# Performance work log

Measured on AMD Instinct MI355X. Metric: run time of the kernel, lower is better.

Reference implementation:

```python
import jax, jax.numpy as jnp
import numpy as np

OPS = jnp.array([[1,1,1],[1,1,-1],[1,-1,1],[1,-1,-1],[-1,1,1],[-1,1,-1],[-1,-1,1],[-1,-1,-1]], dtype=jnp.float32)  # [8,3] sign flips per eigenvector column

B, N, FN, FE, E = 1, 512, 8, 1, 32
D0 = 6 + FN  # layer-0 node embedding dim: framed (x,v) = 6 dims + node features


def setup_inputs() -> dict:
    key = jax.random.key(0)
    ks = jax.random.split(key, 24)
    rn = lambda k, shp, s=0.1: jax.random.normal(k, shp, jnp.float32) * s
    inp = {
        'node_feat': jax.random.normal(ks[0], (B, N, FN), jnp.float32),
        'edge_feat': jax.random.normal(ks[1], (B, N, N, FE), jnp.float32),
        'x': jax.random.normal(ks[2], (B, N, 3), jnp.float32),
        'v': jax.random.normal(ks[3], (B, N, 3), jnp.float32),
        # GNN layer 0 (input node dim D0)
        'e0_w1': rn(ks[4], (FE + 2 * D0, E)), 'e0_b1': jnp.zeros((E,), jnp.float32),
        'e0_w2': rn(ks[5], (E, E)), 'e0_b2': jnp.zeros((E,), jnp.float32),
        'n0_w1': rn(ks[6], (D0 + E, E)), 'n0_b1': jnp.zeros((E,), jnp.float32),
        'n0_w2': rn(ks[7], (E, E)), 'n0_b2': jnp.zeros((E,), jnp.float32),
        # GNN layer 1 (input node dim E)
        'e1_w1': rn(ks[8], (FE + 2 * E, E)), 'e1_b1': jnp.zeros((E,), jnp.float32),
        'e1_w2': rn(ks[9], (E, E)), 'e1_b2': jnp.zeros((E,), jnp.float32),
        'n1_w1': rn(ks[10], (E + E, E)), 'n1_b1': jnp.zeros((E,), jnp.float32),
        'n1_w2': rn(ks[11], (E, E)), 'n1_b2': jnp.zeros((E,), jnp.float32),
        # decoder: relu -> Linear(E,E) -> relu -> Linear(E,6)
        'dec_w1': rn(ks[12], (E, E)), 'dec_b1': jnp.zeros((E,), jnp.float32),
        'dec_w2': rn(ks[13], (E, 6)), 'dec_b2': jnp.zeros((6,), jnp.float32),
        # v_coef: relu -> Linear(E,E) -> relu -> Linear(E,1)
        'vc_w1': rn(ks[14], (E, E)), 'vc_b1': jnp.zeros((E,), jnp.float32),
        'vc_w2': rn(ks[15], (E, 1)), 'vc_b2': jnp.zeros((1,), jnp.float32),
    }
    return inp


def _gnn_layer(h, edge_feat, ew1, eb1, ew2, eb2, nw1, nb1, nw2, nb2):
    # h: [B,N,d]; edge_feat: [B,N,N,Fe]
    # Torch builds concat([edge_feat, h_j, h_i]) per (i,j) pair; we split W1 rows
    # to avoid materializing the [B,N,N,Fe+2d] concat (same math).
    Fe = edge_feat.shape[-1]
    d = h.shape[-1]
    pre_e = edge_feat @ ew1[:Fe]          # [B,N,N,E]
    pre_j = h @ ew1[Fe:Fe + d]            # [B,N,E], indexed by j
    pre_i = h @ ew1[Fe + d:]              # [B,N,E], indexed by i
    m = jax.nn.relu(pre_e + pre_j[:, None, :, :] + pre_i[:, :, None, :] + eb1)
    m = jax.nn.relu(m @ ew2 + eb2)        # [B,N,N,E]
    agg = m.sum(axis=2)                   # sum over neighbors j -> [B,N,E]
    dn = jax.nn.relu(h @ nw1[:d] + agg @ nw1[d:] + nb1)
    return dn @ nw2 + nb2                 # [B,N,E]


def reference(node_feat, edge_feat, x, v,
              e0_w1, e0_b1, e0_w2, e0_b2, n0_w1, n0_b1, n0_w2, n0_b2,
              e1_w1, e1_b1, e1_w2, e1_b2, n1_w1, n1_b1, n1_w2, n1_b2,
              dec_w1, dec_b1, dec_w2, dec_b2, vc_w1, vc_b1, vc_w2, vc_b2):
    # ---- create_frame (PCA frame averaging) ----
    center = x.mean(axis=1, keepdims=True)                 # [B,1,3]
    xc = x - center
    R = jnp.einsum('bni,bnj->bij', xc, xc)                 # [B,3,3]
    _, Vv = jnp.linalg.eigh(R)                             # eigenvectors, ascending (like torch.symeig)
    F_ops = jax.lax.stop_gradient(OPS[None, :, None, :] * Vv[:, None, :, :])  # [B,8,3,3]
    center = jax.lax.stop_gradient(center)
    xc = x - center
    fx = jnp.einsum('boji,bnj->obni', F_ops, xc)           # [8,B,N,3] (F_ops^T applied)
    fv = jnp.einsum('boji,bnj->obni', F_ops, v)            # [8,B,N,3]
    nf = jnp.broadcast_to(node_feat[None], (8,) + node_feat.shape)
    h0 = jnp.concatenate([fx, fv, nf], axis=-1)            # [8,B,N,6+FN]

    l0 = (e0_w1, e0_b1, e0_w2, e0_b2, n0_w1, n0_b1, n0_w2, n0_b2)
    l1 = (e1_w1, e1_b1, e1_w2, e1_b2, n1_w1, n1_b1, n1_w2, n1_b2)
    frames = []
    for i in range(8):  # small fixed frame count; loop keeps N^2 intermediates per-frame
        hi = _gnn_layer(h0[i], edge_feat, *l0)
        hi = _gnn_layer(hi, edge_feat, *l1)
        frames.append(hi)
    h_out = jnp.stack(frames)                              # [8,B,N,E]

    # ---- decoder + invert_frame ----
    s = jax.nn.relu(jax.nn.relu(h_out) @ dec_w1 + dec_b1)
    spatial_out = s @ dec_w2 + dec_b2                      # [8,B,N,6]
    so = jnp.transpose(spatial_out, (1, 0, 2, 3))          # [B,8,N,6]
    dx = jnp.einsum('boij,bonj->bni', F_ops, so[..., :3]) / 8.0
    dv = jnp.einsum('boij,bonj->bni', F_ops, so[..., 3:]) / 8.0

    h_mean = h_out.mean(axis=0)                            # [B,N,E]
    coef = jax.nn.relu(jax.nn.relu(h_mean) @ vc_w1 + vc_b1) @ vc_w2 + vc_b2  # [B,N,1]
    v_out = v + dv
    x_out = x + v_out * coef + dx
    return (h_mean, edge_feat, x_out, v_out)
```

## Files before the change

### kernel.cpp

```cpp
#include <hip/hip_runtime.h>
#include <hip/hip_bf16.h>
#include <hip/hip_fp16.h>
#include <math.h>

#define NN 512

typedef _Float16 f16x8 __attribute__((ext_vector_type(8)));
typedef float    f32x4 __attribute__((ext_vector_type(4)));

__device__ __forceinline__ void compute_frame(const float* __restrict__ x,
                                              float* __restrict__ sFR,
                                              double (*red)[9]) {
    const int t = threadIdx.x;
    double s[9] = {0,0,0,0,0,0,0,0,0};
    for (int n = t; n < NN; n += 256) {
        double X = x[n*3+0], Y = x[n*3+1], Z = x[n*3+2];
        s[0]+=X; s[1]+=Y; s[2]+=Z;
        s[3]+=X*X; s[4]+=X*Y; s[5]+=X*Z; s[6]+=Y*Y; s[7]+=Y*Z; s[8]+=Z*Z;
    }
    #pragma unroll
    for (int m = 1; m < 64; m <<= 1) {
        #pragma unroll
        for (int q = 0; q < 9; ++q) s[q] += __shfl_xor(s[q], m);
    }
    const int wave = t >> 6, lane = t & 63;
    if (lane == 0) {
        #pragma unroll
        for (int q = 0; q < 9; ++q) red[wave][q] = s[q];
    }
    __syncthreads();
    if (t == 0) {
        double S[9];
        #pragma unroll
        for (int q = 0; q < 9; ++q) S[q] = red[0][q]+red[1][q]+red[2][q]+red[3][q];
        double cx = S[0]/512.0, cy = S[1]/512.0, cz = S[2]/512.0;
        double A[3][3];
        A[0][0]=S[3]-512.0*cx*cx; A[0][1]=S[4]-512.0*cx*cy; A[0][2]=S[5]-512.0*cx*cz;
        A[1][1]=S[6]-512.0*cy*cy; A[1][2]=S[7]-512.0*cy*cz; A[2][2]=S[8]-512.0*cz*cz;
        A[1][0]=A[0][1]; A[2][0]=A[0][2]; A[2][1]=A[1][2];
        double V[3][3] = {{1,0,0},{0,1,0},{0,0,1}};
        for (int sweep = 0; sweep < 8; ++sweep) {
            double off = fabs(A[0][1]) + fabs(A[0][2]) + fabs(A[1][2]);
            double dia = fabs(A[0][0]) + fabs(A[1][1]) + fabs(A[2][2]);
            if (off < 1e-14 * (dia + 1e-300)) break;
            for (int p = 0; p < 3; ++p) for (int q = p+1; q < 3; ++q) {
                double apq = A[p][q];
                if (fabs(apq) < 1e-300) continue;
                double tau = (A[q][q] - A[p][p]) / (2.0 * apq);
                double tt = (tau >= 0 ? 1.0 : -1.0) / (fabs(tau) + sqrt(1.0 + tau*tau));
                double cc = 1.0 / sqrt(1.0 + tt*tt), ss = tt * cc;
                A[p][p] = A[p][p] - tt * apq;
                A[q][q] = A[q][q] + tt * apq;
                A[p][q] = 0.0; A[q][p] = 0.0;
                for (int k = 0; k < 3; ++k) if (k != p && k != q) {
                    double akp = A[k][p], akq = A[k][q];
                    A[k][p] = cc*akp - ss*akq; A[p][k] = A[k][p];
                    A[k][q] = ss*akp + cc*akq; A[q][k] = A[k][q];
                }
                for (int k = 0; k < 3; ++k) {
                    double vkp = V[k][p], vkq = V[k][q];
                    V[k][p] = cc*vkp - ss*vkq;
                    V[k][q] = ss*vkp + cc*vkq;
                }
            }
        }
        double ev[3] = {A[0][0], A[1][1], A[2][2]};
        int idx[3] = {0,1,2};
        for (int a = 0; a < 2; ++a) for (int b = a+1; b < 3; ++b)
            if (ev[idx[b]] < ev[idx[a]]) { int tmp = idx[a]; idx[a] = idx[b]; idx[b] = tmp; }
        sFR[0] = (float)cx; sFR[1] = (float)cy; sFR[2] = (float)cz;
        for (int r = 0; r < 3; ++r)
            for (int c = 0; c < 3; ++c)
                sFR[3 + r*3 + c] = (float)V[r][idx[c]];
    }
    __syncthreads();
}

__global__ void __launch_bounds__(256) pre0_kernel(
    const float* __restrict__ x, const float* __restrict__ v,
    const float* __restrict__ nf,
    const float* __restrict__ e0w1, const float* __restrict__ e0b1,
    const float* __restrict__ e0w2, const float* __restrict__ e1w1,
    const float* __restrict__ e1w2,
    const float* __restrict__ edge,
    float* __restrict__ FRg, float* __restrict__ H0,
    _Float16* __restrict__ PJF, _Float16* __restrict__ PIH,
    _Float16* __restrict__ WEH0, _Float16* __restrict__ WEH1,
    _Float16* __restrict__ W2F0, _Float16* __restrict__ W2F1,
    float* __restrict__ out_edge)
{
    __shared__ double red[4][9];
    __shared__ float sFR[12];
    const int t = threadIdx.x;
    const int b = blockIdx.x;

    compute_frame(x, sFR, red);

    ((float2*)out_edge)[b * 256 + t] = ((const float2*)edge)[b * 256 + t];

    if (b == 0) {
        const int lane = t & 63, wv = t >> 6;
        if (t < 12) FRg[t] = sFR[t];
        const int l15 = lane & 15, kb = (lane >> 4) * 8;
        if (wv == 1) {
            #pragma unroll
            for (int e = 0; e < 8; ++e) {
                W2F0[lane*16 + e]     = (_Float16)e0w2[(kb+e)*32 + l15];
                W2F0[lane*16 + 8 + e] = (_Float16)e0w2[(kb+e)*32 + l15 + 16];
            }
        } else if (wv == 2) {
            #pragma unroll
            for (int e = 0; e < 8; ++e) {
                W2F1[lane*16 + e]     = (_Float16)e1w2[(kb+e)*32 + l15];
                W2F1[lane*16 + 8 + e] = (_Float16)e1w2[(kb+e)*32 + l15 + 16];
            }
        } else if (wv == 3 && lane < 32) {
            WEH0[lane] = (_Float16)e0w1[lane];
            WEH1[lane] = (_Float16)e1w1[lane];
        }
    }

    const int c = t & 31;
    const int row = b * 8 + (t >> 5);
    const int o = row >> 9, j = row & 511;
    float hrow[14];
    float xc0 = x[j*3+0] - sFR[0], xc1 = x[j*3+1] - sFR[1], xc2 = x[j*3+2] - sFR[2];
    float v0 = v[j*3+0], v1 = v[j*3+1], v2 = v[j*3+2];
    #pragma unroll
    for (int i = 0; i < 3; ++i) {
        float sgn = ((o >> (2 - i)) & 1) ? -1.f : 1.f;
        float px = sFR[3 + 0*3 + i]*xc0 + sFR[3 + 1*3 + i]*xc1 + sFR[3 + 2*3 + i]*xc2;
        float pv = sFR[3 + 0*3 + i]*v0  + sFR[3 + 1*3 + i]*v1  + sFR[3 + 2*3 + i]*v2;
        hrow[i]     = sgn * px;
        hrow[3 + i] = sgn * pv;
    }
    #pragma unroll
    for (int k = 0; k < 8; ++k) hrow[6 + k] = nf[j*8 + k];
    if (c < 14) H0[row * 14 + c] = hrow[c];
    float pj = 0.f, pi = e0b1[c];
    #pragma unroll
    for (int k = 0; k < 14; ++k) {
        pj = fmaf(hrow[k], e0w1[(1 + k) * 32 + c], pj);
        pi = fmaf(hrow[k], e0w1[(15 + k) * 32 + c], pi);
    }
    PIH[row * 32 + c] = (_Float16)pi;
    const int fl = (j & 15) | ((c >> 3) << 4);
    PJF[(((o << 5) + (j >> 4)) * 64 + fl) * 8 + (c & 7)] = (_Float16)pj;
}

template<int D, bool NEXT>
__global__ void __launch_bounds__(256, 4) edge_kernel(
    const _Float16* __restrict__ PJF,
    const _Float16* __restrict__ PIH,
    const _Float16* __restrict__ WEH,
    const _Float16* __restrict__ W2F,
    const float* __restrict__ edge,
    const float* __restrict__ h,
    const float* __restrict__ eb2,
    const float* __restrict__ nw1,
    const float* __restrict__ nb1,
    const float* __restrict__ nw2,
    const float* __restrict__ nb2,
    float* __restrict__ hout,
    const float* __restrict__ ew1n,
    const float* __restrict__ eb1n,
    _Float16* __restrict__ PJFn,
    _Float16* __restrict__ PIn)
{
    const int t = threadIdx.x;
    const int wv = t >> 6, lane = t & 63;
    const int o = blockIdx.x >> 8;
    const int i0 = (blockIdx.x & 255) << 1;
    const int i = i0 + (wv & 1);
    const int jh = wv >> 1;
    const int row = (o << 9) | i;
    const int l15 = lane & 15;
    const int kbase = (lane >> 4) * 8;

    __shared__ float sAgg[4][32];

    const f16x8 pi8 = *(const f16x8*)(PIH + row * 32 + kbase);
    const f16x8 we8 = *(const f16x8*)(WEH + kbase);
    const f16x8 bfrag0 = *(const f16x8*)(W2F + lane * 16);
    const f16x8 bfrag1 = *(const f16x8*)(W2F + lane * 16 + 8);
    const float b2v0 = eb2[l15], b2v1 = eb2[l15 + 16];
    const f16x8 z8 = {0,0,0,0,0,0,0,0};
    const f32x4 z4 = {0.f, 0.f, 0.f, 0.f};
    const f32x4 bias0 = {b2v0, b2v0, b2v0, b2v0};
    const f32x4 bias1 = {b2v1, b2v1, b2v1, b2v1};
    f32x4 aggv0 = z4, aggv1 = z4;

    const float* edge_i = edge + (i << 9) + (jh << 8);
    const _Float16* pjw = PJF + (size_t)o * 16384 + ((jh << 4) * 64 + lane) * 8;

    f16x8 pjA[8]; float ehA[8];
    #pragma unroll
    for (int u = 0; u < 8; ++u) {
        pjA[u] = *(const f16x8*)(pjw + u * 512);
        ehA[u] = edge_i[u * 16 + l15];
    }
    f16x8 pjB[8]; float ehB[8];
    #pragma unroll
    for (int u = 0; u < 8; ++u) {
        pjB[u] = *(const f16x8*)(pjw + (8 + u) * 512);
        ehB[u] = edge_i[(8 + u) * 16 + l15];
    }

    #pragma unroll
    for (int u = 0; u < 8; ++u) {
        const _Float16 eh = (_Float16)ehA[u];
        const f16x8 e8 = {eh, eh, eh, eh, eh, eh, eh, eh};
        f16x8 m = e8 * we8 + (pjA[u] + pi8);
        m = __builtin_elementwise_max(m, z8);
        f32x4 c0 = __builtin_amdgcn_mfma_f32_16x16x32_f16(m, bfrag0, z4, 0, 0, 0);
        aggv0 += __builtin_elementwise_max(c0 + bias0, z4);
        f32x4 c1 = __builtin_amdgcn_mfma_f32_16x16x32_f16(m, bfrag1, z4, 0, 0, 0);
        aggv1 += __builtin_elementwise_max(c1 + bias1, z4);
    }
    #pragma unroll
    for (int u = 0; u < 8; ++u) {
        const _Float16 eh = (_Float16)ehB[u];
        const f16x8 e8 = {eh, eh, eh, eh, eh, eh, eh, eh};
        f16x8 m = e8 * we8 + (pjB[u] + pi8);
        m = __builtin_elementwise_max(m, z8);
        f32x4 c0 = __builtin_amdgcn_mfma_f32_16x16x32_f16(m, bfrag0, z4, 0, 0, 0);
        aggv0 += __builtin_elementwise_max(c0 + bias0, z4);
        f32x4 c1 = __builtin_amdgcn_mfma_f32_16x16x32_f16(m, bfrag1, z4, 0, 0, 0);
        aggv1 += __builtin_elementwise_max(c1 + bias1, z4);
    }
    float agg0 = (aggv0[0] + aggv0[1]) + (aggv0[2] + aggv0[3]);
    float agg1 = (aggv1[0] + aggv1[1]) + (aggv1[2] + aggv1[3]);

    agg0 += __shfl_xor(agg0, 16); agg0 += __shfl_xor(agg0, 32);
    agg1 += __shfl_xor(agg1, 16); agg1 += __shfl_xor(agg1, 32);
    if (lane < 16) { sAgg[wv][l15] = agg0; sAgg[wv][16 + l15] = agg1; }
    __syncthreads();
    if (wv >= 2) return;

    const int c2 = lane & 31;
    const float red2 = sAgg[wv][c2] + sAgg[wv + 2][c2];
    const float* hr = h + row * D;
    float acc = nb1[c2];
    #pragma unroll
    for (int k = 0; k < D; ++k) acc = fmaf(hr[k], nw1[k * 32 + c2], acc);
    #pragma unroll
    for (int k = 0; k < 32; ++k)
        acc = fmaf(__shfl(red2, k, 32), nw1[(D + k) * 32 + c2], acc);
    const float dn = fmaxf(acc, 0.f);
    float outv = nb2[c2];
    #pragma unroll
    for (int k = 0; k < 32; ++k)
        outv = fmaf(__shfl(dn, k, 32), nw2[k * 32 + c2], outv);
    if (lane < 32) hout[row * 32 + c2] = outv;

    if (NEXT) {
        float pj1 = 0.f, pi1 = eb1n[c2];
        #pragma unroll
        for (int k = 0; k < 32; ++k) {
            const float hk = __shfl(outv, k, 32);
            pj1 = fmaf(hk, ew1n[(1 + k) * 32 + c2], pj1);
            pi1 = fmaf(hk, ew1n[(33 + k) * 32 + c2], pi1);
        }
        if (lane < 32) {
            PIn[row * 32 + c2] = (_Float16)pi1;
            const int fl = (i & 15) | ((c2 >> 3) << 4);
            PJFn[(((o << 5) + (i >> 4)) * 64 + fl) * 8 + (c2 & 7)] = (_Float16)pj1;
        }
    }
}

__global__ void __launch_bounds__(256) decfinal_kernel(
    const float* __restrict__ h2,
    const float* __restrict__ w1, const float* __restrict__ b1,
    const float* __restrict__ w2,
    const float* __restrict__ b2,
    const float* __restrict__ x, const float* __restrict__ v,
    const float* __restrict__ FR,
    const float* __restrict__ vw1, const float* __restrict__ vb1,
    const float* __restrict__ vw2, const float* __restrict__ vb2,
    float* __restrict__ out_hmean, float* __restrict__ out_x,
    float* __restrict__ out_v)
{
    const int n = blockIdx.x;
    const int t = threadIdx.x;
    const int wv = t >> 6, lane = t & 63;
    const int c = lane & 31;
    __shared__ float sSo[8][6];

    #pragma unroll
    for (int q = 0; q < 2; ++q) {
        const int o = (wv << 1) | q;
        const int row = (o << 9) | n;
        float rh = fmaxf(h2[row * 32 + c], 0.f);
        float acc = b1[c];
        #pragma unroll
        for (int k = 0; k < 32; ++k)
            acc = fmaf(__shfl(rh, k, 32), w1[k * 32 + c], acc);
        float s = fmaxf(acc, 0.f);
        #pragma unroll
        for (int m = 0; m < 6; ++m) {
            float p = s * w2[c * 6 + m];
            p += __shfl_xor(p, 1); p += __shfl_xor(p, 2); p += __shfl_xor(p, 4);
            p += __shfl_xor(p, 8); p += __shfl_xor(p, 16);
            if (lane == 0) sSo[o][m] = p + b2[m];
        }
    }
    __syncthreads();
    if (wv) return;

    float hm = 0.f;
    #pragma unroll
    for (int o = 0; o < 8; ++o) hm += h2[((o << 9) | n) * 32 + c];
    hm *= 0.125f;
    if (lane < 32) out_hmean[n * 32 + c] = hm;
    float rh = fmaxf(hm, 0.f);
    float acc = vb1[c];
    #pragma unroll
    for (int k = 0; k < 32; ++k)
        acc = fmaf(__shfl(rh, k, 32), vw1[k * 32 + c], acc);
    float t1 = fmaxf(acc, 0.f);
    float p = t1 * vw2[c];
    p += __shfl_xor(p, 1); p += __shfl_xor(p, 2); p += __shfl_xor(p, 4);
    p += __shfl_xor(p, 8); p += __shfl_xor(p, 16);
    float coef = p + vb2[0];
    if (lane < 3) {
        int i = lane;
        float dx = 0.f, dv = 0.f;
        #pragma unroll
        for (int o = 0; o < 8; ++o) {
            #pragma unroll
            for (int j = 0; j < 3; ++j) {
                float sgn = ((o >> (2 - j)) & 1) ? -1.f : 1.f;
                float f = sgn * FR[3 + i * 3 + j];
                dx = fmaf(f, sSo[o][j], dx);
                dv = fmaf(f, sSo[o][3 + j], dv);
            }
        }
        dx *= 0.125f; dv *= 0.125f;
        float vout = v[n * 3 + i] + dv;
        out_v[n * 3 + i] = vout;
        out_x[n * 3 + i] = x[n * 3 + i] + vout * coef + dx;
    }
}

extern "C" void kernel_launch(void* const* d_in, const int* in_sizes, int n_in,
                              void* d_out, int out_size, void* d_ws, size_t ws_size,
                              hipStream_t stream) {
    const float* node_feat = (const float*)d_in[0];
    const float* edge      = (const float*)d_in[1];
    const float* x         = (const float*)d_in[2];
    const float* v         = (const float*)d_in[3];
    const float* e0_w1 = (const float*)d_in[4];
    const float* e0_b1 = (const float*)d_in[5];
    const float* e0_w2 = (const float*)d_in[6];
    const float* e0_b2 = (const float*)d_in[7];
    const float* n0_w1 = (const float*)d_in[8];
    const float* n0_b1 = (const float*)d_in[9];
    const float* n0_w2 = (const float*)d_in[10];
    const float* n0_b2 = (const float*)d_in[11];
    const float* e1_w1 = (const float*)d_in[12];
    const float* e1_b1 = (const float*)d_in[13];
    const float* e1_w2 = (const float*)d_in[14];
    const float* e1_b2 = (const float*)d_in[15];
    const float* n1_w1 = (const float*)d_in[16];
    const float* n1_b1 = (const float*)d_in[17];
    const float* n1_w2 = (const float*)d_in[18];
    const float* n1_b2 = (const float*)d_in[19];
    const float* dec_w1 = (const float*)d_in[20];
    const float* dec_b1 = (const float*)d_in[21];
    const float* dec_w2 = (const float*)d_in[22];
    const float* dec_b2 = (const float*)d_in[23];
    const float* vc_w1 = (const float*)d_in[24];
    const float* vc_b1 = (const float*)d_in[25];
    const float* vc_w2 = (const float*)d_in[26];
    const float* vc_b2 = (const float*)d_in[27];

    char* wsb = (char*)d_ws;
    float* out = (float*)d_out;

    float*    FR   = (float*)wsb;
    float*    H0   = (float*)(wsb + 256);
    float*    HA   = (float*)(wsb + 256 + 229376);
    float*    HB   = (float*)(wsb + 256 + 229376 + 524288);
    char*     p    = wsb + 256 + 229376 + 524288 + 524288;
    _Float16* PJF0 = (_Float16*)p;            p += 262144;
    _Float16* PIH0 = (_Float16*)p;            p += 262144;
    _Float16* PJF1 = (_Float16*)p;            p += 262144;
    _Float16* PIH1 = (_Float16*)p;            p += 262144;
    _Float16* WEH0 = (_Float16*)p;            p += 256;
    _Float16* WEH1 = (_Float16*)p;            p += 256;
    _Float16* W2F0 = (_Float16*)p;            p += 2048;
    _Float16* W2F1 = (_Float16*)p;            p += 2048;

    pre0_kernel<<<512, 256, 0, stream>>>(x, v, node_feat,
                                         e0_w1, e0_b1, e0_w2, e1_w1, e1_w2,
                                         edge, FR, H0, PJF0, PIH0,
                                         WEH0, WEH1, W2F0, W2F1, out + 16384);
    edge_kernel<14, true><<<2048, 256, 0, stream>>>(
        PJF0, PIH0, WEH0, W2F0, edge, H0, e0_b2, n0_w1, n0_b1, n0_w2, n0_b2,
        HA, e1_w1, e1_b1, PJF1, PIH1);
    edge_kernel<32, false><<<2048, 256, 0, stream>>>(
        PJF1, PIH1, WEH1, W2F1, edge, HA, e1_b2, n1_w1, n1_b1, n1_w2, n1_b2,
        HB, nullptr, nullptr, nullptr, nullptr);
    decfinal_kernel<<<512, 256, 0, stream>>>(HB, dec_w1, dec_b1, dec_w2, dec_b2,
                                             x, v, FR, vc_w1, vc_b1, vc_w2, vc_b2,
                                             out, out + 278528, out + 280064);
}
```

Baseline: 159.5 us.

## Use closed-form 3x3 eigensolver and raise edge kernel occupancy

Replaces the iterative Jacobi eigen-decomposition in the frame computation with a closed-form trigonometric solver for symmetric 3x3 matrices, with eigenvectors taken from cross products. In the edge kernel it drops the explicit two-batch register prefetch of PJF and edge values in favour of a single unrolled 16-step loop, and raises the launch-bounds minimum blocks per CU from 4 to 8. The aim is a shorter serial single-thread eigen section and more resident waves to hide memory latency. The closed-form solver may differ numerically or in eigenvector sign from the Jacobi result, and the tighter register budget could cause spills or lose the explicit load overlap.

```diff
diff --git a/kernel.cpp b/kernel.cpp
--- a/kernel.cpp
+++ b/kernel.cpp
@@ -7,6 +7,63 @@
 
 typedef _Float16 f16x8 __attribute__((ext_vector_type(8)));
 typedef float    f32x4 __attribute__((ext_vector_type(4)));
+
+__device__ __forceinline__ void eig3_sym(const double A[3][3], double V[3][3]) {
+    const double a00 = A[0][0], a11 = A[1][1], a22 = A[2][2];
+    const double a01 = A[0][1], a02 = A[0][2], a12 = A[1][2];
+    double p1 = a01*a01 + a02*a02 + a12*a12;
+    double lam0, lam2;
+    if (p1 < 1e-30) {
+        double d[3] = {a00, a11, a22};
+        int idx[3] = {0, 1, 2};
+        for (int a = 0; a < 2; ++a) for (int b = a+1; b < 3; ++b)
+            if (d[idx[b]] < d[idx[a]]) { int t = idx[a]; idx[a] = idx[b]; idx[b] = t; }
+        for (int r = 0; r < 3; ++r) for (int c = 0; c < 3; ++c)
+            V[r][c] = (r == idx[c]) ? 1.0 : 0.0;
+        return;
+    }
+    double q = (a00 + a11 + a22) / 3.0;
+    double b00 = a00 - q, b11 = a11 - q, b22 = a22 - q;
+    double p2 = b00*b00 + b11*b11 + b22*b22 + 2.0 * p1;
+    double p = sqrt(p2 / 6.0);
+    double inv_p = 1.0 / p;
+    double c00 = b00*inv_p, c11 = b11*inv_p, c22 = b22*inv_p;
+    double c01 = a01*inv_p, c02 = a02*inv_p, c12 = a12*inv_p;
+    double detB = c00*(c11*c22 - c12*c12) - c01*(c01*c22 - c12*c02)
+                + c02*(c01*c12 - c11*c02);
+    double r = detB * 0.5;
+    r = fmin(1.0, fmax(-1.0, r));
+    double phi = acos(r) / 3.0;
+    lam2 = q + 2.0 * p * cos(phi);
+    lam0 = q + 2.0 * p * cos(phi + 2.0943951023931953);
+    double vs[2][3]; double lams[2] = {lam0, lam2};
+    for (int e = 0; e < 2; ++e) {
+        double l = lams[e];
+        double r0[3] = {a00 - l, a01, a02};
+        double r1[3] = {a01, a11 - l, a12};
+        double r2[3] = {a02, a12, a22 - l};
+        double c0[3] = {r0[1]*r1[2]-r0[2]*r1[1], r0[2]*r1[0]-r0[0]*r1[2], r0[0]*r1[1]-r0[1]*r1[0]};
+        double c1[3] = {r0[1]*r2[2]-r0[2]*r2[1], r0[2]*r2[0]-r0[0]*r2[2], r0[0]*r2[1]-r0[1]*r2[0]};
+        double c2[3] = {r1[1]*r2[2]-r1[2]*r2[1], r1[2]*r2[0]-r1[0]*r2[2], r1[0]*r2[1]-r1[1]*r2[0]};
+        double n0 = c0[0]*c0[0]+c0[1]*c0[1]+c0[2]*c0[2];
+        double n1 = c1[0]*c1[0]+c1[1]*c1[1]+c1[2]*c1[2];
+        double n2 = c2[0]*c2[0]+c2[1]*c2[1]+c2[2]*c2[2];
+        double* best = c0; double nb = n0;
+        if (n1 > nb) { best = c1; nb = n1; }
+        if (n2 > nb) { best = c2; nb = n2; }
+        double inv = 1.0 / sqrt(nb);
+        vs[e][0] = best[0]*inv; vs[e][1] = best[1]*inv; vs[e][2] = best[2]*inv;
+    }
+    double vm[3] = {vs[1][1]*vs[0][2]-vs[1][2]*vs[0][1],
+                    vs[1][2]*vs[0][0]-vs[1][0]*vs[0][2],
+                    vs[1][0]*vs[0][1]-vs[1][1]*vs[0][0]};
+    double nm = 1.0 / sqrt(vm[0]*vm[0]+vm[1]*vm[1]+vm[2]*vm[2]);
+    for (int rr = 0; rr < 3; ++rr) {
+        V[rr][0] = vs[0][rr];
+        V[rr][1] = vm[rr]*nm;
+        V[rr][2] = vs[1][rr];
+    }
+}
 
 __device__ __forceinline__ void compute_frame(const float* __restrict__ x,
                                               float* __restrict__ sFR,
@@ -38,40 +95,12 @@
         A[0][0]=S[3]-512.0*cx*cx; A[0][1]=S[4]-512.0*cx*cy; A[0][2]=S[5]-512.0*cx*cz;
         A[1][1]=S[6]-512.0*cy*cy; A[1][2]=S[7]-512.0*cy*cz; A[2][2]=S[8]-512.0*cz*cz;
         A[1][0]=A[0][1]; A[2][0]=A[0][2]; A[2][1]=A[1][2];
-        double V[3][3] = {{1,0,0},{0,1,0},{0,0,1}};
-        for (int sweep = 0; sweep < 8; ++sweep) {
-            double off = fabs(A[0][1]) + fabs(A[0][2]) + fabs(A[1][2]);
-            double dia = fabs(A[0][0]) + fabs(A[1][1]) + fabs(A[2][2]);
-            if (off < 1e-14 * (dia + 1e-300)) break;
-            for (int p = 0; p < 3; ++p) for (int q = p+1; q < 3; ++q) {
-                double apq = A[p][q];
-                if (fabs(apq) < 1e-300) continue;
-                double tau = (A[q][q] - A[p][p]) / (2.0 * apq);
-                double tt = (tau >= 0 ? 1.0 : -1.0) / (fabs(tau) + sqrt(1.0 + tau*tau));
-                double cc = 1.0 / sqrt(1.0 + tt*tt), ss = tt * cc;
-                A[p][p] = A[p][p] - tt * apq;
-                A[q][q] = A[q][q] + tt * apq;
-                A[p][q] = 0.0; A[q][p] = 0.0;
-                for (int k = 0; k < 3; ++k) if (k != p && k != q) {
-                    double akp = A[k][p], akq = A[k][q];
-                    A[k][p] = cc*akp - ss*akq; A[p][k] = A[k][p];
-                    A[k][q] = ss*akp + cc*akq; A[q][k] = A[k][q];
-                }
-                for (int k = 0; k < 3; ++k) {
-                    double vkp = V[k][p], vkq = V[k][q];
-                    V[k][p] = cc*vkp - ss*vkq;
-                    V[k][q] = ss*vkp + cc*vkq;
-                }
-            }
-        }
-        double ev[3] = {A[0][0], A[1][1], A[2][2]};
-        int idx[3] = {0,1,2};
-        for (int a = 0; a < 2; ++a) for (int b = a+1; b < 3; ++b)
-            if (ev[idx[b]] < ev[idx[a]]) { int tmp = idx[a]; idx[a] = idx[b]; idx[b] = tmp; }
+        double V[3][3];
+        eig3_sym(A, V);
         sFR[0] = (float)cx; sFR[1] = (float)cy; sFR[2] = (float)cz;
         for (int r = 0; r < 3; ++r)
             for (int c = 0; c < 3; ++c)
-                sFR[3 + r*3 + c] = (float)V[r][idx[c]];
+                sFR[3 + r*3 + c] = (float)V[r][c];
     }
     __syncthreads();
 }
@@ -149,7 +178,7 @@
 }
 
 template<int D, bool NEXT>
-__global__ void __launch_bounds__(256, 4) edge_kernel(
+__global__ void __launch_bounds__(256, 8) edge_kernel(
     const _Float16* __restrict__ PJF,
     const _Float16* __restrict__ PIH,
     const _Float16* __restrict__ WEH,
@@ -193,35 +222,12 @@
     const float* edge_i = edge + (i << 9) + (jh << 8);
     const _Float16* pjw = PJF + (size_t)o * 16384 + ((jh << 4) * 64 + lane) * 8;
 
-    f16x8 pjA[8]; float ehA[8];
-    #pragma unroll
-    for (int u = 0; u < 8; ++u) {
-        pjA[u] = *(const f16x8*)(pjw + u * 512);
-        ehA[u] = edge_i[u * 16 + l15];
-    }
-    f16x8 pjB[8]; float ehB[8];
-    #pragma unroll
-    for (int u = 0; u < 8; ++u) {
-        pjB[u] = *(const f16x8*)(pjw + (8 + u) * 512);
-        ehB[u] = edge_i[(8 + u) * 16 + l15];
-    }
-
-    #pragma unroll
-    for (int u = 0; u < 8; ++u) {
-        const _Float16 eh = (_Float16)ehA[u];
+    #pragma unroll
+    for (int u = 0; u < 16; ++u) {
+        const f16x8 pj8 = *(const f16x8*)(pjw + u * 512);
+        const _Float16 eh = (_Float16)edge_i[u * 16 + l15];
         const f16x8 e8 = {eh, eh, eh, eh, eh, eh, eh, eh};
-        f16x8 m = e8 * we8 + (pjA[u] + pi8);
-        m = __builtin_elementwise_max(m, z8);
-        f32x4 c0 = __builtin_amdgcn_mfma_f32_16x16x32_f16(m, bfrag0, z4, 0, 0, 0);
-        aggv0 += __builtin_elementwise_max(c0 + bias0, z4);
-        f32x4 c1 = __builtin_amdgcn_mfma_f32_16x16x32_f16(m, bfrag1, z4, 0, 0, 0);
-        aggv1 += __builtin_elementwise_max(c1 + bias1, z4);
-    }
-    #pragma unroll
-    for (int u = 0; u < 8; ++u) {
-        const _Float16 eh = (_Float16)ehB[u];
-        const f16x8 e8 = {eh, eh, eh, eh, eh, eh, eh, eh};
-        f16x8 m = e8 * we8 + (pjB[u] + pi8);
+        f16x8 m = e8 * we8 + (pj8 + pi8);
         m = __builtin_elementwise_max(m, z8);
         f32x4 c0 = __builtin_amdgcn_mfma_f32_16x16x32_f16(m, bfrag0, z4, 0, 0, 0);
         aggv0 += __builtin_elementwise_max(c0 + bias0, z4);
```

Result: no change. 157.1 us (-1.5%).
